# Kernel tuning notes

Hardware: AMD Instinct MI355X
Metric: run time of the kernel (lower is better)

The kernel has to match this reference:

```python
import jax, jax.numpy as jnp
import numpy as np

B, F, T, K = 16, 256, 2048, 20
TEMP = 0.5
EPS = 1e-8  # torch cosine_similarity eps


def setup_inputs() -> dict:
    key = jax.random.key(0)
    k1, k2, k3 = jax.random.split(key, 3)
    z = jax.random.normal(k1, (B, F, T), dtype=jnp.float32)
    c = jax.random.normal(k2, (B, F, T + 1), dtype=jnp.float32)
    # torch: torch.randint(0, full_len - 1, size=(B, T * K))  -> values in [0, T-2]
    negative_inds = jax.random.randint(k3, (B, T * K), 0, T - 1, dtype=jnp.int64)
    return {"z": z, "c": c, "negative_inds": negative_inds}


def reference(z, c, negative_inds):
    # ---- _generate_negatives ----
    # z: [B, F, T] -> flat rows [B*T, F]
    z_flat = jnp.transpose(z, (0, 2, 1)).reshape(-1, F)
    # per-batch offset i*T (torch adds it in-place for i in 1..B-1)
    inds = negative_inds + (jnp.arange(B, dtype=negative_inds.dtype) * T)[:, None]
    negatives = z_flat[inds.reshape(-1)].reshape(B, T, K, F)

    # ---- _calculate_similarity ----
    c_t = jnp.transpose(c[..., 1:], (0, 2, 1))[:, :, None, :]  # [B, T, 1, F] (drop start token)
    z_t = jnp.transpose(z, (0, 2, 1))[:, :, None, :]           # [B, T, 1, F]
    neg_is_pos = jnp.all(c_t == negatives, axis=-1)            # [B, T, K]
    targets = jnp.concatenate([c_t, negatives], axis=-2)       # [B, T, K+1, F]

    num = jnp.sum(z_t * targets, axis=-1)                      # [B, T, K+1]
    denom = jnp.maximum(
        jnp.linalg.norm(z_t, axis=-1) * jnp.linalg.norm(targets, axis=-1), EPS
    )
    logits = (num / denom) / TEMP                              # [B, T, K+1]

    # mask negatives that exactly equal the positive (wav2vec2-style)
    pad = jnp.zeros_like(neg_is_pos[..., :1])
    full_mask = jnp.concatenate([pad, neg_is_pos], axis=-1)    # [B, T, K+1]
    logits = jnp.where(full_mask, -jnp.inf, logits)

    return logits.reshape(-1, K + 1)                           # [B*T, K+1]
```

## Files before the change

### kernel.cpp

```cpp
#include <hip/hip_runtime.h>
#include <hip/hip_fp16.h>
#include <math.h>

#define B_ 16
#define F_ 256
#define T_ 2048
#define K_ 20
#define OUTK 21
#define NPAIR 11
#define CTOFF (B_ * T_ * F_ * 2)

typedef _Float16 half2v __attribute__((ext_vector_type(2)));

__device__ __forceinline__ half2v h2(unsigned u) { return __builtin_bit_cast(half2v, u); }
__device__ __forceinline__ float fdot2f(unsigned a, unsigned b, float c) {
#if __has_builtin(__builtin_amdgcn_fdot2)
    return __builtin_amdgcn_fdot2(h2(a), h2(b), c, false);
#else
    half2v x = h2(a), y = h2(b);
    return fmaf((float)x[1], (float)y[1], fmaf((float)x[0], (float)y[0], c));
#endif
}

__global__ __launch_bounds__(256) void transpose_norm2_kernel(
    const float* __restrict__ z, const float* __restrict__ c,
    ushort* __restrict__ zth, ushort* __restrict__ cth)
{
    __shared__ float tile[256][33];
    __shared__ float sc[32];
    int which = blockIdx.z;
    const float* src = which ? c : z;
    ushort* dst = which ? cth : zth;
    int Lsrc = which ? (T_ + 1) : T_;
    int co   = which;

    int b  = blockIdx.y;
    int t0 = blockIdx.x * 32;
    const float* srcb = src + (size_t)b * F_ * Lsrc;
    int tl = threadIdx.x & 31;
    int fl = threadIdx.x >> 5;
#pragma unroll
    for (int i = 0; i < 32; ++i) {
        int f = i * 8 + fl;
        tile[f][tl] = srcb[(size_t)f * Lsrc + (t0 + tl + co)];
    }
    __syncthreads();
    if (threadIdx.x < 32) {
        float s = 0.f;
#pragma unroll 8
        for (int f = 0; f < 256; ++f) { float v = tile[f][threadIdx.x]; s += v * v; }
        float n = sqrtf(s);
        sc[threadIdx.x] = (n > 0.f) ? (1.0f / n) : 0.f;
    }
    __syncthreads();
    int l   = threadIdx.x & 127;
    int rhi = threadIdx.x >> 7;
#pragma unroll
    for (int j2 = 0; j2 < 16; ++j2) {
        int row = j2 * 2 + rhi;
        float s  = sc[row];
        float a  = tile[2 * l][row] * s;
        float bb = tile[2 * l + 1][row] * s;
        unsigned u = ((unsigned)__half_as_ushort(__float2half(bb)) << 16)
                   |  (unsigned)__half_as_ushort(__float2half(a));
        unsigned* drow = (unsigned*)(dst + ((size_t)b * T_ + t0 + row) * F_);
        drow[l] = u;
    }
}

__device__ __forceinline__ float dpp_half_sum(float x) {
    x += __int_as_float(__builtin_amdgcn_mov_dpp(__float_as_int(x), 0x111, 0xF, 0xF, true));
    x += __int_as_float(__builtin_amdgcn_mov_dpp(__float_as_int(x), 0x112, 0xF, 0xF, true));
    x += __int_as_float(__builtin_amdgcn_mov_dpp(__float_as_int(x), 0x114, 0xF, 0xF, true));
    x += __int_as_float(__builtin_amdgcn_mov_dpp(__float_as_int(x), 0x118, 0xF, 0xF, true));
    x += __int_as_float(__builtin_amdgcn_mov_dpp(__float_as_int(x), 0x142, 0xF, 0xF, true));
    return x;
}

__global__ __launch_bounds__(256, 6) void sim_kernel(
    const ushort* __restrict__ zth, const ushort* __restrict__ cth,
    const int* __restrict__ inds, float* __restrict__ out)
{
    __shared__ float sd[128];
    int i = blockIdx.x;
    int b = (i & 7) | ((i >= 4096) ? 8 : 0);
    int wid = threadIdx.x >> 6;
    int t = (((i >> 3) & 511) << 2) + wid;
    int lane = threadIdx.x & 63;
    int hl = lane & 31;
    int hi = lane >> 5;
    int bt = __builtin_amdgcn_readfirstlane((b << 11) + t);

    const int* myinds = inds + bt * K_;
    int idxv = myinds[(lane < K_) ? lane : 0];

    const uint4* zrow = (const uint4*)(zth + (size_t)bt * F_);
    const uint4* crow = (const uint4*)(cth + (size_t)bt * F_);
    uint4 zv = zrow[hl];
    uint4 cv = crow[hl];

    const char* tbl = (const char*)zth;
    unsigned zbase = (unsigned)(b << 11) * 512u;
    unsigned laneoff = (unsigned)hl * 16u;
    unsigned cbyte = (unsigned)CTOFF + (unsigned)bt * 512u;

    uint4 tv[NPAIR];
    {
        unsigned ohi = zbase + (unsigned)__builtin_amdgcn_readlane(idxv, 0) * 512u;
        tv[0] = *(const uint4*)(tbl + ((hi ? ohi : cbyte) + laneoff));
    }
#pragma unroll
    for (int p = 1; p < NPAIR; ++p) {
        unsigned ilo = (unsigned)__builtin_amdgcn_readlane(idxv, 2 * p - 1);
        unsigned ihi = (unsigned)__builtin_amdgcn_readlane(idxv, (p == 10) ? 19 : 2 * p);
        unsigned off = zbase + (hi ? ihi : ilo) * 512u + laneoff;
        tv[p] = *(const uint4*)(tbl + off);
    }

    __builtin_amdgcn_sched_barrier(0);

    float dz[NPAIR];
#pragma unroll
    for (int p = 0; p < NPAIR; ++p) {
        float d = fdot2f(tv[p].x, zv.x, 0.f);
        d = fdot2f(tv[p].y, zv.y, d);
        d = fdot2f(tv[p].z, zv.z, d);
        d = fdot2f(tv[p].w, zv.w, d);
        dz[p] = d;
    }

    unsigned mb = 0;
#pragma unroll
    for (int p = 0; p < NPAIR; ++p) {
        unsigned long long ball = __ballot(tv[p].x == cv.x);
        unsigned blo = (unsigned)ball, bhi = (unsigned)(ball >> 32);
        if (blo == 0xFFFFFFFFu || bhi == 0xFFFFFFFFu) {
            bool full = (tv[p].x == cv.x) && (tv[p].y == cv.y) &&
                        (tv[p].z == cv.z) && (tv[p].w == cv.w);
            unsigned long long b2 = __ballot(full);
            if ((unsigned)b2 == 0xFFFFFFFFu)          mb |= 1u << (2 * p);
            if ((unsigned)(b2 >> 32) == 0xFFFFFFFFu)  mb |= 1u << (2 * p + 1);
        }
    }
    mb &= ~1u;

#pragma unroll
    for (int p = 0; p < NPAIR; ++p) dz[p] = dpp_half_sum(dz[p]);

    int slotbase = wid * 32 + hi;
    if (hl == 31) {
#pragma unroll
        for (int p = 0; p < NPAIR; ++p) sd[slotbase + 2 * p] = dz[p];
    }

    if (lane < OUTK) {
        float v = sd[wid * 32 + lane] * 2.0f;
        if ((mb >> lane) & 1u) v = -INFINITY;
        out[(size_t)bt * OUTK + lane] = v;
    }
}

extern "C" void kernel_launch(void* const* d_in, const int* in_sizes, int n_in,
                              void* d_out, int out_size, void* d_ws, size_t ws_size,
                              hipStream_t stream)
{
    const float* z    = (const float*)d_in[0];
    const float* c    = (const float*)d_in[1];
    const int*   inds = (const int*)d_in[2];
    float* out = (float*)d_out;

    char* ws = (char*)d_ws;
    size_t th_bytes = (size_t)B_ * T_ * F_ * sizeof(ushort);
    ushort* zth = (ushort*)ws;
    ushort* cth = (ushort*)(ws + th_bytes);

    dim3 tb(256), tg(T_ / 32, B_, 2);
    transpose_norm2_kernel<<<tg, tb, 0, stream>>>(z, c, zth, cth);
    sim_kernel<<<dim3(B_ * T_ / 4), dim3(256), 0, stream>>>(zth, cth, inds, out);
}
```

Before: 44.68 us.

## Store gathered negatives as FP8 and compute positive logit in prep kernel

The prep kernel now loads z and c tiles together. It computes the positive cosine logit exactly in fp32 and writes it directly to the output. It also emits an fp16 copy of z plus normalized FP8 (e4m3) copies of z and c. The similarity kernel gathers the 20 negatives from the FP8 table, halving the random-gather bytes, and dots them against the fp16 z row in fp32. Occupancy is raised to 8 waves. The cost is much lower precision on the negative logits, which may exceed tolerance. The equality mask now compares FP8-quantized rows, so distinct vectors that round to the same bytes could be masked wrongly.

```diff
diff --git a/kernel.cpp b/kernel.cpp
--- a/kernel.cpp
+++ b/kernel.cpp
@@ -7,64 +7,130 @@
 #define T_ 2048
 #define K_ 20
 #define OUTK 21
-#define NPAIR 11
-#define CTOFF (B_ * T_ * F_ * 2)
+#define NPAIR 10
 
 typedef _Float16 half2v __attribute__((ext_vector_type(2)));
-
-__device__ __forceinline__ half2v h2(unsigned u) { return __builtin_bit_cast(half2v, u); }
-__device__ __forceinline__ float fdot2f(unsigned a, unsigned b, float c) {
-#if __has_builtin(__builtin_amdgcn_fdot2)
-    return __builtin_amdgcn_fdot2(h2(a), h2(b), c, false);
+typedef float v2f __attribute__((ext_vector_type(2)));
+
+#if __has_builtin(__builtin_amdgcn_cvt_pk_f32_fp8) && __has_builtin(__builtin_amdgcn_cvt_pk_fp8_f32)
+#define HW_FP8 1
 #else
-    half2v x = h2(a), y = h2(b);
-    return fmaf((float)x[1], (float)y[1], fmaf((float)x[0], (float)y[0], c));
-#endif
-}
-
-__global__ __launch_bounds__(256) void transpose_norm2_kernel(
+#define HW_FP8 0
+#endif
+
+#if !HW_FP8
+__device__ __forceinline__ float dec_fp8(unsigned v) {
+    unsigned s = (v >> 7) & 1, e = (v >> 3) & 15, m = v & 7;
+    float r = e ? __uint_as_float(((e + 120u) << 23) | (m << 20))
+                : (float)m * 0.001953125f;
+    return s ? -r : r;
+}
+__device__ __forceinline__ unsigned enc_fp8(float x) {
+    unsigned bits = __float_as_uint(x);
+    unsigned s = bits >> 31;
+    unsigned a = bits & 0x7fffffffu;
+    float ax = __uint_as_float(a);
+    unsigned r;
+    if (ax < 0.015625f) {
+        r = (unsigned)(int)(ax * 512.f + 0.5f);
+    } else {
+        int e = (int)(a >> 23) - 127;
+        unsigned m = a & 0x7fffffu;
+        unsigned keep = m >> 20, rest = m & 0xFFFFFu;
+        keep += (rest > 0x80000u) || (rest == 0x80000u && (keep & 1));
+        if (keep == 8) { keep = 0; ++e; }
+        r = ((unsigned)(e + 7) << 3) | keep;
+    }
+    return (s << 7) | r;
+}
+#endif
+
+__device__ __forceinline__ unsigned pack_fp8x4(float a0, float a1, float a2, float a3) {
+#if HW_FP8
+    int u = 0;
+    u = __builtin_amdgcn_cvt_pk_fp8_f32(a0, a1, u, false);
+    u = __builtin_amdgcn_cvt_pk_fp8_f32(a2, a3, u, true);
+    return (unsigned)u;
+#else
+    return enc_fp8(a0) | (enc_fp8(a1) << 8) | (enc_fp8(a2) << 16) | (enc_fp8(a3) << 24);
+#endif
+}
+template <bool HI>
+__device__ __forceinline__ v2f unpk_fp8(unsigned u) {
+#if HW_FP8
+    return __builtin_amdgcn_cvt_pk_f32_fp8((int)u, HI);
+#else
+    v2f r; unsigned x = HI ? (u >> 16) : u;
+    r[0] = dec_fp8(x & 0xFF); r[1] = dec_fp8((x >> 8) & 0xFF);
+    return r;
+#endif
+}
+
+__global__ __launch_bounds__(256) void prep_kernel(
     const float* __restrict__ z, const float* __restrict__ c,
-    ushort* __restrict__ zth, ushort* __restrict__ cth)
+    ushort* __restrict__ zth, unsigned char* __restrict__ zf8,
+    unsigned char* __restrict__ cf8, float* __restrict__ out)
 {
-    __shared__ float tile[256][33];
-    __shared__ float sc[32];
-    int which = blockIdx.z;
-    const float* src = which ? c : z;
-    ushort* dst = which ? cth : zth;
-    int Lsrc = which ? (T_ + 1) : T_;
-    int co   = which;
-
+    __shared__ float tz[256][33];
+    __shared__ float tc[256][33];
+    __shared__ float scz[32], scc[32];
     int b  = blockIdx.y;
     int t0 = blockIdx.x * 32;
-    const float* srcb = src + (size_t)b * F_ * Lsrc;
+    const float* zb = z + (size_t)b * F_ * T_;
+    const float* cb = c + (size_t)b * F_ * (T_ + 1);
     int tl = threadIdx.x & 31;
     int fl = threadIdx.x >> 5;
 #pragma unroll
     for (int i = 0; i < 32; ++i) {
         int f = i * 8 + fl;
-        tile[f][tl] = srcb[(size_t)f * Lsrc + (t0 + tl + co)];
+        tz[f][tl] = zb[(size_t)f * T_ + t0 + tl];
+    }
+#pragma unroll
+    for (int i = 0; i < 32; ++i) {
+        int f = i * 8 + fl;
+        tc[f][tl] = cb[(size_t)f * (T_ + 1) + t0 + tl + 1];
     }
     __syncthreads();
     if (threadIdx.x < 32) {
-        float s = 0.f;
+        float zn = 0.f, cn = 0.f, zc = 0.f;
 #pragma unroll 8
-        for (int f = 0; f < 256; ++f) { float v = tile[f][threadIdx.x]; s += v * v; }
-        float n = sqrtf(s);
-        sc[threadIdx.x] = (n > 0.f) ? (1.0f / n) : 0.f;
+        for (int f = 0; f < 256; ++f) {
+            float a = tz[f][threadIdx.x], d = tc[f][threadIdx.x];
+            zn = fmaf(a, a, zn); cn = fmaf(d, d, cn); zc = fmaf(a, d, zc);
+        }
+        float nz_ = sqrtf(zn), nc_ = sqrtf(cn);
+        scz[threadIdx.x] = (nz_ > 0.f) ? (1.0f / nz_) : 0.f;
+        scc[threadIdx.x] = (nc_ > 0.f) ? (1.0f / nc_) : 0.f;
+        int bt = (b << 11) + t0 + threadIdx.x;
+        out[(size_t)bt * OUTK] = (zc / fmaxf(nz_ * nc_, 1e-8f)) * 2.0f;
     }
     __syncthreads();
-    int l   = threadIdx.x & 127;
-    int rhi = threadIdx.x >> 7;
-#pragma unroll
-    for (int j2 = 0; j2 < 16; ++j2) {
-        int row = j2 * 2 + rhi;
-        float s  = sc[row];
-        float a  = tile[2 * l][row] * s;
-        float bb = tile[2 * l + 1][row] * s;
-        unsigned u = ((unsigned)__half_as_ushort(__float2half(bb)) << 16)
-                   |  (unsigned)__half_as_ushort(__float2half(a));
-        unsigned* drow = (unsigned*)(dst + ((size_t)b * T_ + t0 + row) * F_);
-        drow[l] = u;
+    {
+        int l = threadIdx.x & 127, rhi = threadIdx.x >> 7;
+#pragma unroll
+        for (int j2 = 0; j2 < 16; ++j2) {
+            int row = j2 * 2 + rhi;
+            float s = scz[row];
+            float a  = tz[2 * l][row] * s;
+            float bb = tz[2 * l + 1][row] * s;
+            unsigned u = ((unsigned)__half_as_ushort(__float2half(bb)) << 16)
+                       |  (unsigned)__half_as_ushort(__float2half(a));
+            ((unsigned*)(zth + ((size_t)b * T_ + t0 + row) * F_))[l] = u;
+        }
+    }
+    {
+        int j = threadIdx.x & 63, r4 = threadIdx.x >> 6;
+#pragma unroll
+        for (int it = 0; it < 8; ++it) {
+            int row = it * 4 + r4;
+            float sz_ = scz[row], sc_ = scc[row];
+            unsigned uz = pack_fp8x4(tz[4 * j][row] * sz_, tz[4 * j + 1][row] * sz_,
+                                     tz[4 * j + 2][row] * sz_, tz[4 * j + 3][row] * sz_);
+            unsigned uc = pack_fp8x4(tc[4 * j][row] * sc_, tc[4 * j + 1][row] * sc_,
+                                     tc[4 * j + 2][row] * sc_, tc[4 * j + 3][row] * sc_);
+            ((unsigned*)(zf8 + ((size_t)b * T_ + t0 + row) * F_))[j] = uz;
+            ((unsigned*)(cf8 + ((size_t)b * T_ + t0 + row) * F_))[j] = uc;
+        }
     }
 }
 
@@ -77,9 +143,10 @@
     return x;
 }
 
-__global__ __launch_bounds__(256, 6) void sim_kernel(
-    const ushort* __restrict__ zth, const ushort* __restrict__ cth,
-    const int* __restrict__ inds, float* __restrict__ out)
+__global__ __launch_bounds__(256, 8) void sim_kernel(
+    const ushort* __restrict__ zth, const unsigned char* __restrict__ zf8,
+    const unsigned char* __restrict__ cf8, const int* __restrict__ inds,
+    float* __restrict__ out)
 {
     __shared__ float sd[128];
     int i = blockIdx.x;
@@ -94,66 +161,74 @@
     const int* myinds = inds + bt * K_;
     int idxv = myinds[(lane < K_) ? lane : 0];
 
-    const uint4* zrow = (const uint4*)(zth + (size_t)bt * F_);
-    const uint4* crow = (const uint4*)(cth + (size_t)bt * F_);
-    uint4 zv = zrow[hl];
-    uint4 cv = crow[hl];
-
-    const char* tbl = (const char*)zth;
-    unsigned zbase = (unsigned)(b << 11) * 512u;
-    unsigned laneoff = (unsigned)hl * 16u;
-    unsigned cbyte = (unsigned)CTOFF + (unsigned)bt * 512u;
-
-    uint4 tv[NPAIR];
+    uint4 zv  = ((const uint4*)(zth + (size_t)bt * F_))[hl];
+    uint2 cv8 = ((const uint2*)(cf8 + (size_t)bt * F_))[hl];
+
+    const char* tbl8 = (const char*)zf8;
+    unsigned zbase8  = (unsigned)(b << 11) * 256u;
+    unsigned laneoff = (unsigned)hl * 8u;
+
+    uint2 tv[NPAIR];
+#pragma unroll
+    for (int p = 0; p < NPAIR; ++p) {
+        unsigned ilo = (unsigned)__builtin_amdgcn_readlane(idxv, 2 * p);
+        unsigned ihi = (unsigned)__builtin_amdgcn_readlane(idxv, 2 * p + 1);
+        unsigned off = zbase8 + (hi ? ihi : ilo) * 256u + laneoff;
+        tv[p] = *(const uint2*)(tbl8 + off);
+    }
+
+    __builtin_amdgcn_sched_barrier(0);
+
+    float zf[8];
     {
-        unsigned ohi = zbase + (unsigned)__builtin_amdgcn_readlane(idxv, 0) * 512u;
-        tv[0] = *(const uint4*)(tbl + ((hi ? ohi : cbyte) + laneoff));
-    }
-#pragma unroll
-    for (int p = 1; p < NPAIR; ++p) {
-        unsigned ilo = (unsigned)__builtin_amdgcn_readlane(idxv, 2 * p - 1);
-        unsigned ihi = (unsigned)__builtin_amdgcn_readlane(idxv, (p == 10) ? 19 : 2 * p);
-        unsigned off = zbase + (hi ? ihi : ilo) * 512u + laneoff;
-        tv[p] = *(const uint4*)(tbl + off);
-    }
-
-    __builtin_amdgcn_sched_barrier(0);
+        unsigned uu[4] = {zv.x, zv.y, zv.z, zv.w};
+#pragma unroll
+        for (int q = 0; q < 4; ++q) {
+            half2v h = __builtin_bit_cast(half2v, uu[q]);
+            zf[2 * q] = (float)h[0]; zf[2 * q + 1] = (float)h[1];
+        }
+    }
 
     float dz[NPAIR];
 #pragma unroll
     for (int p = 0; p < NPAIR; ++p) {
-        float d = fdot2f(tv[p].x, zv.x, 0.f);
-        d = fdot2f(tv[p].y, zv.y, d);
-        d = fdot2f(tv[p].z, zv.z, d);
-        d = fdot2f(tv[p].w, zv.w, d);
+        v2f t01 = unpk_fp8<false>(tv[p].x);
+        v2f t23 = unpk_fp8<true >(tv[p].x);
+        v2f t45 = unpk_fp8<false>(tv[p].y);
+        v2f t67 = unpk_fp8<true >(tv[p].y);
+        float d = zf[0] * t01[0];
+        d = fmaf(zf[1], t01[1], d);
+        d = fmaf(zf[2], t23[0], d);
+        d = fmaf(zf[3], t23[1], d);
+        d = fmaf(zf[4], t45[0], d);
+        d = fmaf(zf[5], t45[1], d);
+        d = fmaf(zf[6], t67[0], d);
+        d = fmaf(zf[7], t67[1], d);
         dz[p] = d;
     }
 
     unsigned mb = 0;
 #pragma unroll
     for (int p = 0; p < NPAIR; ++p) {
-        unsigned long long ball = __ballot(tv[p].x == cv.x);
+        unsigned long long ball = __ballot(tv[p].x == cv8.x);
         unsigned blo = (unsigned)ball, bhi = (unsigned)(ball >> 32);
         if (blo == 0xFFFFFFFFu || bhi == 0xFFFFFFFFu) {
-            bool full = (tv[p].x == cv.x) && (tv[p].y == cv.y) &&
-                        (tv[p].z == cv.z) && (tv[p].w == cv.w);
+            bool full = (tv[p].x == cv8.x) && (tv[p].y == cv8.y);
             unsigned long long b2 = __ballot(full);
-            if ((unsigned)b2 == 0xFFFFFFFFu)          mb |= 1u << (2 * p);
-            if ((unsigned)(b2 >> 32) == 0xFFFFFFFFu)  mb |= 1u << (2 * p + 1);
-        }
-    }
-    mb &= ~1u;
+            if ((unsigned)b2 == 0xFFFFFFFFu)          mb |= 1u << (1 + 2 * p);
+            if ((unsigned)(b2 >> 32) == 0xFFFFFFFFu)  mb |= 1u << (2 + 2 * p);
+        }
+    }
 
 #pragma unroll
     for (int p = 0; p < NPAIR; ++p) dz[p] = dpp_half_sum(dz[p]);
 
-    int slotbase = wid * 32 + hi;
     if (hl == 31) {
 #pragma unroll
-        for (int p = 0; p < NPAIR; ++p) sd[slotbase + 2 * p] = dz[p];
-    }
-
-    if (lane < OUTK) {
+        for (int p = 0; p < NPAIR; ++p) sd[wid * 32 + 1 + 2 * p + hi] = dz[p];
+    }
+
+    if (lane >= 1 && lane < OUTK) {
         float v = sd[wid * 32 + lane] * 2.0f;
         if ((mb >> lane) & 1u) v = -INFINITY;
         out[(size_t)bt * OUTK + lane] = v;
@@ -170,11 +245,13 @@
     float* out = (float*)d_out;
 
     char* ws = (char*)d_ws;
-    size_t th_bytes = (size_t)B_ * T_ * F_ * sizeof(ushort);
+    size_t f16_bytes = (size_t)B_ * T_ * F_ * sizeof(ushort);
+    size_t f8_bytes  = (size_t)B_ * T_ * F_;
     ushort* zth = (ushort*)ws;
-    ushort* cth = (ushort*)(ws + th_bytes);
-
-    dim3 tb(256), tg(T_ / 32, B_, 2);
-    transpose_norm2_kernel<<<tg, tb, 0, stream>>>(z, c, zth, cth);
-    sim_kernel<<<dim3(B_ * T_ / 4), dim3(256), 0, stream>>>(zth, cth, inds, out);
-}
+    unsigned char* zf8 = (unsigned char*)(ws + f16_bytes);
+    unsigned char* cf8 = (unsigned char*)(ws + f16_bytes + f8_bytes);
+
+    dim3 tb(256), tg(T_ / 32, B_);
+    prep_kernel<<<tg, tb, 0, stream>>>(z, c, zth, zf8, cf8, out);
+    sim_kernel<<<dim3(B_ * T_ / 4), dim3(256), 0, stream>>>(zth, zf8, cf8, inds, out);
+}
```

New measurement: 52.24 us. 16.9% more time.
